# Optimization experiments

Measured on AMD Instinct MI355X. Metric: run time of the kernel, lower is better.

Reference implementation:

```python
import jax, jax.numpy as jnp
import numpy as np

NUM_EXPERTS = 4
HIDDEN = 768
INTER = 192  # expert_inter; gate_up projects to 2*INTER
TOKENS = 131072


def setup_inputs() -> dict:
    key = jax.random.key(0)
    k1, k2, k3, k4 = jax.random.split(key, 4)
    hidden = jax.random.normal(k1, (TOKENS, HIDDEN), dtype=jnp.float32)
    expert_ids = jax.random.randint(k2, (TOKENS,), 0, NUM_EXPERTS, dtype=jnp.int64)
    gate_up = jax.random.normal(k3, (NUM_EXPERTS, HIDDEN, 2 * INTER), dtype=jnp.float32) * 0.02
    down = jax.random.normal(k4, (NUM_EXPERTS, INTER, HIDDEN), dtype=jnp.float32) * 0.02
    return {"hidden": hidden, "expert_ids": expert_ids, "gate_up": gate_up, "down": down}


def reference(hidden, expert_ids, gate_up, down):
    # Math-equivalent to scatter -> per-expert SwiGLU MLP -> gather back:
    # for each token t with expert e = expert_ids[t]:
    #   out[t] = (silu(x_t @ gate_up[e][:, :F]) * (x_t @ gate_up[e][:, F:])) @ down[e]
    # With E=4 (small), compute per-expert dense and select via one-hot; this is
    # jit-friendly (static shapes) and exactly matches the per-token math.
    E = gate_up.shape[0]
    F = down.shape[1]
    onehot = (expert_ids[None, :] == jnp.arange(E)[:, None]).astype(hidden.dtype)  # [E, T]
    gu = jnp.einsum('th,ehf->etf', hidden, gate_up)      # [E, T, 2F]
    gate, up = gu[..., :F], gu[..., F:]                  # [E, T, F]
    act = jax.nn.silu(gate) * up                         # SwiGLU
    out = jnp.einsum('etf,efh,et->th', act, down, onehot)  # select token's own expert
    return out
```

## Files before the change

### kernel.cpp

```cpp
#include <hip/hip_runtime.h>
#include <hip/hip_bf16.h>

#define NE 4
#define HD 768
#define F2 384
#define F1 192
#define NT 131072
#define TT 128

typedef __attribute__((ext_vector_type(8))) short bf16x8;
typedef __attribute__((ext_vector_type(4))) float f32x4;
typedef __attribute__((ext_vector_type(4))) unsigned int u32x4;

#define LA0 0u
#define LA1 8192u
#define LB0 16384u
#define LB1 40960u
#define LACT 0u
#define LB2 49152u
#define LTOK 73728u
#define SMEM_BYTES 74240

#define WS_BUCKET_OFF 256
#define WS_B1IMG_OFF (WS_BUCKET_OFF + NE*NT*4)
#define WS_DNIMG_OFF (WS_B1IMG_OFF + NE*24*24576)

__device__ __forceinline__ unsigned short f2bf(float x) {
    unsigned int u = __float_as_uint(x);
    return (unsigned short)((u + 0x7fffu + ((u >> 16) & 1u)) >> 16);
}
__device__ __forceinline__ unsigned int pk2(float a, float b) {
    unsigned int ua = __float_as_uint(a), ub = __float_as_uint(b);
    unsigned int lo = (ua + 0x7fffu + ((ua >> 16) & 1u)) >> 16;
    unsigned int hi = (ub + 0x7fffu + ((ub >> 16) & 1u)) & 0xffff0000u;
    return lo | hi;
}
#define GLL(srcp, ldsoff) \
    __builtin_amdgcn_global_load_lds((const __attribute__((address_space(1))) void*)(srcp), \
        (__attribute__((address_space(3))) void*)(smem + (ldsoff)), 16, 0, 0)

__global__ void route_kernel(const int* __restrict__ ids, int* __restrict__ counts,
                             int* __restrict__ bucket) {
    __shared__ int lc[NE];
    __shared__ int lb[NE];
    int tid = threadIdx.x;
    if (tid < NE) lc[tid] = 0;
    __syncthreads();
    int t = blockIdx.x * blockDim.x + tid;
    int e = ids[t];
    int rank = atomicAdd(&lc[e], 1);
    __syncthreads();
    if (tid < NE) lb[tid] = atomicAdd(&counts[tid], lc[tid]);
    __syncthreads();
    bucket[e * NT + lb[e] + rank] = t;
}

__global__ void b1img_kernel(const float* __restrict__ gu, unsigned short* __restrict__ b1img) {
    int idx = blockIdx.x * 256 + threadIdx.x;
    int L = idx % 1536;
    int es = idx / 1536;
    int kstep = es % 24, e = es / 24;
    int colp = L >> 3, slot = L & 7;
    int v = slot ^ (colp & 7);
    int tc = colp * 2 + (v >> 2);
    int kb = kstep * 32 + (v & 3) * 8;
    const float* src = gu + ((size_t)(e * HD + kb)) * F2 + tc;
    unsigned short o[8];
    #pragma unroll
    for (int j = 0; j < 8; ++j) o[j] = f2bf(src[(size_t)j * F2]);
    *(bf16x8*)(b1img + ((size_t)idx) * 8) = *(const bf16x8*)o;
}

__global__ void dnimg_kernel(const float* __restrict__ dn, unsigned short* __restrict__ dnimg) {
    int idx = blockIdx.x * 256 + threadIdx.x;
    int L = idx % 1536;
    int r = idx / 1536;
    int kt = r % 6; r /= 6;
    int half = r & 1; int e = r >> 1;
    int colp = L >> 3, slot = L & 7;
    int v = slot ^ (colp & 7);
    int tc = colp * 2 + (v >> 2);
    int kb = kt * 32 + (v & 3) * 8;
    const float* src = dn + ((size_t)(e * F1 + kb)) * HD + half * 384 + tc;
    unsigned short o[8];
    #pragma unroll
    for (int j = 0; j < 8; ++j) o[j] = f2bf(src[(size_t)j * HD]);
    *(bf16x8*)(dnimg + ((size_t)idx) * 8) = *(const bf16x8*)o;
}

__global__ __launch_bounds__(512, 2)
void moe_kernel(const float* __restrict__ hidden, const int* __restrict__ counts,
                const int* __restrict__ bucket, const unsigned short* __restrict__ b1img,
                const unsigned short* __restrict__ dnimg, float* __restrict__ out)
{
    extern __shared__ __align__(16) unsigned char smem[];

    int rem = blockIdx.x, e, n_e = 0;
    for (e = 0; e < NE; ++e) {
        n_e = counts[e];
        int ntiles = (n_e + TT - 1) >> 7;
        if (rem < ntiles) break;
        rem -= ntiles;
    }
    if (e >= NE) return;
    int t0 = rem << 7;

    int tid = threadIdx.x;
    int lane = tid & 63;
    int w = tid >> 6;
    int rw64 = (w >> 2) << 6;
    int cq = w & 3;
    int lg = lane >> 4;
    int l16 = lane & 15;

    int* tokp = (int*)(smem + LTOK);
    if (tid < TT) {
        int idx = t0 + tid; if (idx >= n_e) idx = n_e - 1;
        tokp[tid] = bucket[e * NT + idx];
    }
    __syncthreads();

    int arow = tid >> 2, kq = tid & 3;
    const float* aptr = hidden + (size_t)tokp[arow] * HD + kq * 8;
    unsigned awb = (unsigned)((tid >> 3) * 128 +
                   (((kq + ((arow & 1) << 2)) ^ ((tid >> 3) & 7)) << 4));

    const unsigned short* gls = b1img + (size_t)e * 24 * 12288 + (w * 3) * 512 + lane * 8;
    unsigned gld = (unsigned)(w * 3) * 1024u;

    const unsigned short* gls2 = dnimg + (size_t)e * 12 * 12288 + (w * 3) * 512 + lane * 8;

    unsigned laneoff = (unsigned)(((l16 >> 1) << 7) +
                       (((lg + ((l16 & 1) << 2)) ^ (l16 >> 1)) << 4));
    unsigned arb[4], brb[6], b2rb[6];
    #pragma unroll
    for (int mt = 0; mt < 4; ++mt)
        arb[mt] = (unsigned)((rw64 + mt * 16) * 64) + laneoff;
    #pragma unroll
    for (int nt = 0; nt < 6; ++nt) {
        int tcb = (nt < 3) ? (cq * 48 + nt * 16) : (192 + cq * 48 + (nt - 3) * 16);
        brb[nt] = (unsigned)(tcb * 64) + laneoff;
        b2rb[nt] = LB2 + (unsigned)((cq * 96 + nt * 16) * 64) + laneoff;
    }

    f32x4 av0, av1;
    auto issueA = [&](int k0) {
        const f32x4* p = (const f32x4*)(aptr + k0);
        av0 = p[0]; av1 = p[1];
    };
    auto writeA = [&](unsigned base) {
        u32x4 vv = {pk2(av0.x,av0.y), pk2(av0.z,av0.w), pk2(av1.x,av1.y), pk2(av1.z,av1.w)};
        *(u32x4*)(smem + base + awb) = vv;
    };

    const f32x4 fzero = {0.f, 0.f, 0.f, 0.f};
    f32x4 acc[4][6];
    #pragma unroll
    for (int mt = 0; mt < 4; ++mt)
        #pragma unroll
        for (int nt = 0; nt < 6; ++nt) acc[mt][nt] = fzero;

    issueA(0);
    #pragma unroll
    for (int i = 0; i < 3; ++i) GLL(gls + i * 512, LB0 + gld + i * 1024u);
    writeA(LA0);
    __syncthreads();

    #pragma unroll 1
    for (int t = 0; t < 24; ++t) {
        unsigned Ab  = (t & 1) ? LA1 : LA0;
        unsigned Bb  = (t & 1) ? LB1 : LB0;
        unsigned Abn = (t & 1) ? LA0 : LA1;
        unsigned Bbn = (t & 1) ? LB0 : LB1;
        if (t < 23) {
            issueA((t + 1) * 32);
            #pragma unroll
            for (int i = 0; i < 3; ++i) GLL(gls + (t + 1) * 12288 + i * 512, Bbn + gld + i * 1024u);
        }

        bf16x8 Af[4];
        #pragma unroll
        for (int mt = 0; mt < 4; ++mt) Af[mt] = *(const bf16x8*)(smem + Ab + arb[mt]);
        __builtin_amdgcn_s_setprio(1);
        #pragma unroll
        for (int nt = 0; nt < 6; ++nt) {
            bf16x8 Bf = *(const bf16x8*)(smem + Bb + brb[nt]);
            #pragma unroll
            for (int mt = 0; mt < 4; ++mt)
                acc[mt][nt] = __builtin_amdgcn_mfma_f32_16x16x32_bf16(Af[mt], Bf, acc[mt][nt], 0, 0, 0);
        }
        __builtin_amdgcn_s_setprio(0);

        if (t < 23) writeA(Abn);
        __syncthreads();
    }

    #pragma unroll
    for (int i = 0; i < 3; ++i) GLL(gls2 + i * 512, LB2 + gld + i * 1024u);

    #pragma unroll
    for (int mt = 0; mt < 4; ++mt)
        #pragma unroll
        for (int nt = 0; nt < 3; ++nt)
            #pragma unroll
            for (int p = 0; p < 4; ++p) {
                float g = acc[mt][nt][p];
                float u = acc[mt][nt + 3][p];
                float s = g / (1.f + __expf(-g));
                int row = rw64 + mt * 16 + 4 * lg + p;
                int f = cq * 48 + nt * 16 + l16;
                int c = f >> 3;
                unsigned b = (unsigned)(LACT + row * 384 + (((c & 24) | ((c & 7) ^ (row & 7))) << 4) + (f & 7) * 2);
                *(unsigned short*)(smem + b) = f2bf(s * u);
            }
    __syncthreads();

    #pragma unroll 1
    for (int half = 0; half < 2; ++half) {
        f32x4 c2[4][6];
        #pragma unroll
        for (int mt = 0; mt < 4; ++mt)
            #pragma unroll
            for (int nt = 0; nt < 6; ++nt) c2[mt][nt] = fzero;

        #pragma unroll 1
        for (int kt = 0; kt < 6; ++kt) {
            int c = kt * 4 + lg;
            unsigned a2sl = (unsigned)(((c & 24) | ((c & 7) ^ (l16 & 7))) << 4);
            bf16x8 A2[4], B2f[6];
            #pragma unroll
            for (int mt = 0; mt < 4; ++mt)
                A2[mt] = *(const bf16x8*)(smem + LACT + (rw64 + mt * 16 + l16) * 384 + a2sl);
            #pragma unroll
            for (int nt = 0; nt < 6; ++nt)
                B2f[nt] = *(const bf16x8*)(smem + b2rb[nt]);
            __syncthreads();

            int nidx = half * 6 + kt + 1;
            if (nidx < 12) {
                #pragma unroll
                for (int i = 0; i < 3; ++i)
                    GLL(gls2 + (size_t)nidx * 12288 + i * 512, LB2 + gld + i * 1024u);
            }

            __builtin_amdgcn_s_setprio(1);
            #pragma unroll
            for (int nt = 0; nt < 6; ++nt)
                #pragma unroll
                for (int mt = 0; mt < 4; ++mt)
                    c2[mt][nt] = __builtin_amdgcn_mfma_f32_16x16x32_bf16(A2[mt], B2f[nt], c2[mt][nt], 0, 0, 0);
            __builtin_amdgcn_s_setprio(0);

            __syncthreads();
        }

        #pragma unroll
        for (int mt = 0; mt < 4; ++mt)
            #pragma unroll
            for (int p = 0; p < 4; ++p) {
                int row = rw64 + mt * 16 + 4 * lg + p;
                if (t0 + row < n_e) {
                    float* orow = out + (size_t)tokp[row] * HD + half * 384 + cq * 96 + l16;
                    #pragma unroll
                    for (int nt = 0; nt < 6; ++nt)
                        orow[nt * 16] = c2[mt][nt][p];
                }
            }
    }
}

extern "C" void kernel_launch(void* const* d_in, const int* in_sizes, int n_in,
                              void* d_out, int out_size, void* d_ws, size_t ws_size,
                              hipStream_t stream) {
    (void)in_sizes; (void)n_in; (void)out_size; (void)ws_size;
    const float* hidden = (const float*)d_in[0];
    const int*   ids    = (const int*)d_in[1];
    const float* gu     = (const float*)d_in[2];
    const float* dn     = (const float*)d_in[3];
    float* out = (float*)d_out;

    char* ws = (char*)d_ws;
    int* counts = (int*)ws;
    int* bucket = (int*)(ws + WS_BUCKET_OFF);
    unsigned short* b1img = (unsigned short*)(ws + WS_B1IMG_OFF);
    unsigned short* dnimg = (unsigned short*)(ws + WS_DNIMG_OFF);

    hipMemsetAsync(d_ws, 0, 64, stream);
    route_kernel<<<NT / 256, 256, 0, stream>>>(ids, counts, bucket);
    b1img_kernel<<<576, 256, 0, stream>>>(gu, b1img);
    dnimg_kernel<<<288, 256, 0, stream>>>(dn, dnimg);
    moe_kernel<<<1028, 512, SMEM_BYTES, stream>>>(hidden, counts, bucket, b1img, dnimg, out);
}
```

Baseline: 324.0 us.

## Deepen weight prefetch to multi-stage LDS ring with manual waitcnt barriers

Replaces the double-buffered B-tile pipeline with a 4-stage LDS ring for the gate_up GEMM and a 3-stage ring for the down GEMM, prefetching two tiles ahead. It also prefetches two A tiles into registers and swaps __syncthreads for explicit s_waitcnt vmcnt plus s_barrier, so outstanding global loads are not drained every iteration. The loops are fully unrolled. LDS use grows to about 120KB and launch bounds drop to one block per CU, so the extra pipeline depth is paid for with lower occupancy.

```diff
diff --git a/kernel.cpp b/kernel.cpp
--- a/kernel.cpp
+++ b/kernel.cpp
@@ -12,14 +12,8 @@
 typedef __attribute__((ext_vector_type(4))) float f32x4;
 typedef __attribute__((ext_vector_type(4))) unsigned int u32x4;
 
-#define LA0 0u
-#define LA1 8192u
-#define LB0 16384u
-#define LB1 40960u
-#define LACT 0u
-#define LB2 49152u
-#define LTOK 73728u
-#define SMEM_BYTES 74240
+#define SMEM_BYTES 123392
+#define LTOK 122880u
 
 #define WS_BUCKET_OFF 256
 #define WS_B1IMG_OFF (WS_BUCKET_OFF + NE*NT*4)
@@ -88,12 +82,16 @@
     *(bf16x8*)(dnimg + ((size_t)idx) * 8) = *(const bf16x8*)o;
 }
 
-__global__ __launch_bounds__(512, 2)
+__global__ __launch_bounds__(512, 1)
 void moe_kernel(const float* __restrict__ hidden, const int* __restrict__ counts,
                 const int* __restrict__ bucket, const unsigned short* __restrict__ b1img,
                 const unsigned short* __restrict__ dnimg, float* __restrict__ out)
 {
     extern __shared__ __align__(16) unsigned char smem[];
+    const unsigned LAo[2] = {0u, 8192u};
+    const unsigned LBo[4] = {16384u, 40960u, 65536u, 90112u};
+    const unsigned LCo[3] = {49152u, 73728u, 98304u};
+    const unsigned LACT = 0u;
 
     int rem = blockIdx.x, e, n_e = 0;
     for (e = 0; e < NE; ++e) {
@@ -125,10 +123,9 @@
     unsigned awb = (unsigned)((tid >> 3) * 128 +
                    (((kq + ((arow & 1) << 2)) ^ ((tid >> 3) & 7)) << 4));
 
-    const unsigned short* gls = b1img + (size_t)e * 24 * 12288 + (w * 3) * 512 + lane * 8;
+    const unsigned short* gls  = b1img + (size_t)e * 24 * 12288 + (w * 3) * 512 + lane * 8;
+    const unsigned short* gls2 = dnimg + (size_t)e * 12 * 12288 + (w * 3) * 512 + lane * 8;
     unsigned gld = (unsigned)(w * 3) * 1024u;
-
-    const unsigned short* gls2 = dnimg + (size_t)e * 12 * 12288 + (w * 3) * 512 + lane * 8;
 
     unsigned laneoff = (unsigned)(((l16 >> 1) << 7) +
                        (((lg + ((l16 & 1) << 2)) ^ (l16 >> 1)) << 4));
@@ -140,19 +137,10 @@
     for (int nt = 0; nt < 6; ++nt) {
         int tcb = (nt < 3) ? (cq * 48 + nt * 16) : (192 + cq * 48 + (nt - 3) * 16);
         brb[nt] = (unsigned)(tcb * 64) + laneoff;
-        b2rb[nt] = LB2 + (unsigned)((cq * 96 + nt * 16) * 64) + laneoff;
-    }
-
-    f32x4 av0, av1;
-    auto issueA = [&](int k0) {
-        const f32x4* p = (const f32x4*)(aptr + k0);
-        av0 = p[0]; av1 = p[1];
-    };
-    auto writeA = [&](unsigned base) {
-        u32x4 vv = {pk2(av0.x,av0.y), pk2(av0.z,av0.w), pk2(av1.x,av1.y), pk2(av1.z,av1.w)};
-        *(u32x4*)(smem + base + awb) = vv;
-    };
-
+        b2rb[nt] = (unsigned)((cq * 96 + nt * 16) * 64) + laneoff;
+    }
+
+    f32x4 avb[2][2];
     const f32x4 fzero = {0.f, 0.f, 0.f, 0.f};
     f32x4 acc[4][6];
     #pragma unroll
@@ -160,43 +148,66 @@
         #pragma unroll
         for (int nt = 0; nt < 6; ++nt) acc[mt][nt] = fzero;
 
-    issueA(0);
-    #pragma unroll
-    for (int i = 0; i < 3; ++i) GLL(gls + i * 512, LB0 + gld + i * 1024u);
-    writeA(LA0);
-    __syncthreads();
-
-    #pragma unroll 1
-    for (int t = 0; t < 24; ++t) {
-        unsigned Ab  = (t & 1) ? LA1 : LA0;
-        unsigned Bb  = (t & 1) ? LB1 : LB0;
-        unsigned Abn = (t & 1) ? LA0 : LA1;
-        unsigned Bbn = (t & 1) ? LB0 : LB1;
-        if (t < 23) {
-            issueA((t + 1) * 32);
-            #pragma unroll
-            for (int i = 0; i < 3; ++i) GLL(gls + (t + 1) * 12288 + i * 512, Bbn + gld + i * 1024u);
+    {
+        const f32x4* p0 = (const f32x4*)(aptr);
+        avb[0][0] = p0[0]; avb[0][1] = p0[1];
+        const f32x4* p1 = (const f32x4*)(aptr + 32);
+        avb[1][0] = p1[0]; avb[1][1] = p1[1];
+        #pragma unroll
+        for (int i = 0; i < 3; ++i) GLL(gls + i * 512, LBo[0] + gld + i * 1024u);
+        #pragma unroll
+        for (int i = 0; i < 3; ++i) GLL(gls + 12288 + i * 512, LBo[1] + gld + i * 1024u);
+        u32x4 vv = {pk2(avb[0][0].x,avb[0][0].y), pk2(avb[0][0].z,avb[0][0].w),
+                    pk2(avb[0][1].x,avb[0][1].y), pk2(avb[0][1].z,avb[0][1].w)};
+        *(u32x4*)(smem + LAo[0] + awb) = vv;
+        asm volatile("s_waitcnt vmcnt(3) lgkmcnt(0)");
+        __builtin_amdgcn_s_barrier();
+        __builtin_amdgcn_sched_barrier(0);
+    }
+
+    #pragma unroll
+    for (int g = 0; g < 24; ++g) {
+        if (g < 22) {
+            const f32x4* p = (const f32x4*)(aptr + (g + 2) * 32);
+            avb[g & 1][0] = p[0]; avb[g & 1][1] = p[1];
+            #pragma unroll
+            for (int i = 0; i < 3; ++i)
+                GLL(gls + (size_t)(g + 2) * 12288 + i * 512, LBo[(g + 2) & 3] + gld + i * 1024u);
         }
 
         bf16x8 Af[4];
         #pragma unroll
-        for (int mt = 0; mt < 4; ++mt) Af[mt] = *(const bf16x8*)(smem + Ab + arb[mt]);
+        for (int mt = 0; mt < 4; ++mt)
+            Af[mt] = *(const bf16x8*)(smem + LAo[g & 1] + arb[mt]);
         __builtin_amdgcn_s_setprio(1);
         #pragma unroll
         for (int nt = 0; nt < 6; ++nt) {
-            bf16x8 Bf = *(const bf16x8*)(smem + Bb + brb[nt]);
+            bf16x8 Bf = *(const bf16x8*)(smem + LBo[g & 3] + brb[nt]);
             #pragma unroll
             for (int mt = 0; mt < 4; ++mt)
                 acc[mt][nt] = __builtin_amdgcn_mfma_f32_16x16x32_bf16(Af[mt], Bf, acc[mt][nt], 0, 0, 0);
         }
         __builtin_amdgcn_s_setprio(0);
 
-        if (t < 23) writeA(Abn);
-        __syncthreads();
-    }
-
-    #pragma unroll
-    for (int i = 0; i < 3; ++i) GLL(gls2 + i * 512, LB2 + gld + i * 1024u);
+        if (g < 23) {
+            f32x4 a0 = avb[(g + 1) & 1][0], a1 = avb[(g + 1) & 1][1];
+            u32x4 vv = {pk2(a0.x,a0.y), pk2(a0.z,a0.w), pk2(a1.x,a1.y), pk2(a1.z,a1.w)};
+            *(u32x4*)(smem + LAo[(g + 1) & 1] + awb) = vv;
+            if (g < 22) asm volatile("s_waitcnt vmcnt(5) lgkmcnt(0)");
+            else        asm volatile("s_waitcnt vmcnt(0) lgkmcnt(0)");
+            __builtin_amdgcn_s_barrier();
+            __builtin_amdgcn_sched_barrier(0);
+        }
+    }
+
+    asm volatile("s_waitcnt lgkmcnt(0)");
+    __builtin_amdgcn_s_barrier();
+    __builtin_amdgcn_sched_barrier(0);
+
+    #pragma unroll
+    for (int i = 0; i < 3; ++i) GLL(gls2 + i * 512, LCo[0] + gld + i * 1024u);
+    #pragma unroll
+    for (int i = 0; i < 3; ++i) GLL(gls2 + 12288 + i * 512, LCo[1] + gld + i * 1024u);
 
     #pragma unroll
     for (int mt = 0; mt < 4; ++mt)
@@ -213,9 +224,11 @@
                 unsigned b = (unsigned)(LACT + row * 384 + (((c & 24) | ((c & 7) ^ (row & 7))) << 4) + (f & 7) * 2);
                 *(unsigned short*)(smem + b) = f2bf(s * u);
             }
-    __syncthreads();
-
-    #pragma unroll 1
+    asm volatile("s_waitcnt vmcnt(3) lgkmcnt(0)");
+    __builtin_amdgcn_s_barrier();
+    __builtin_amdgcn_sched_barrier(0);
+
+    #pragma unroll
     for (int half = 0; half < 2; ++half) {
         f32x4 c2[4][6];
         #pragma unroll
@@ -223,35 +236,37 @@
             #pragma unroll
             for (int nt = 0; nt < 6; ++nt) c2[mt][nt] = fzero;
 
-        #pragma unroll 1
+        #pragma unroll
         for (int kt = 0; kt < 6; ++kt) {
+            const int s = half * 6 + kt;
+            if (s < 10) {
+                #pragma unroll
+                for (int i = 0; i < 3; ++i)
+                    GLL(gls2 + (size_t)(s + 2) * 12288 + i * 512, LCo[(s + 2) % 3] + gld + i * 1024u);
+            }
+
             int c = kt * 4 + lg;
             unsigned a2sl = (unsigned)(((c & 24) | ((c & 7) ^ (l16 & 7))) << 4);
-            bf16x8 A2[4], B2f[6];
+            bf16x8 A2[4];
             #pragma unroll
             for (int mt = 0; mt < 4; ++mt)
                 A2[mt] = *(const bf16x8*)(smem + LACT + (rw64 + mt * 16 + l16) * 384 + a2sl);
-            #pragma unroll
-            for (int nt = 0; nt < 6; ++nt)
-                B2f[nt] = *(const bf16x8*)(smem + b2rb[nt]);
-            __syncthreads();
-
-            int nidx = half * 6 + kt + 1;
-            if (nidx < 12) {
-                #pragma unroll
-                for (int i = 0; i < 3; ++i)
-                    GLL(gls2 + (size_t)nidx * 12288 + i * 512, LB2 + gld + i * 1024u);
-            }
-
             __builtin_amdgcn_s_setprio(1);
             #pragma unroll
-            for (int nt = 0; nt < 6; ++nt)
+            for (int nt = 0; nt < 6; ++nt) {
+                bf16x8 B2f = *(const bf16x8*)(smem + LCo[s % 3] + b2rb[nt]);
                 #pragma unroll
                 for (int mt = 0; mt < 4; ++mt)
-                    c2[mt][nt] = __builtin_amdgcn_mfma_f32_16x16x32_bf16(A2[mt], B2f[nt], c2[mt][nt], 0, 0, 0);
+                    c2[mt][nt] = __builtin_amdgcn_mfma_f32_16x16x32_bf16(A2[mt], B2f, c2[mt][nt], 0, 0, 0);
+            }
             __builtin_amdgcn_s_setprio(0);
 
-            __syncthreads();
+            if (s < 11) {
+                if (s < 10) asm volatile("s_waitcnt vmcnt(3) lgkmcnt(0)");
+                else        asm volatile("s_waitcnt vmcnt(0) lgkmcnt(0)");
+                __builtin_amdgcn_s_barrier();
+                __builtin_amdgcn_sched_barrier(0);
+            }
         }
 
         #pragma unroll
```

New measurement: 287.2 us. 11.4% less time.
